# Performance work log

Measured on AMD Instinct MI355X. Metric: run time of the kernel, lower is better.

The kernel has to match this reference:

```python
import jax, jax.numpy as jnp
import numpy as np


def setup_inputs() -> dict:
    key = jax.random.key(0)
    k1, k2, k3, k4 = jax.random.split(key, 4)
    B, S, DIN, DOUT = 4, 4096, 512, 128
    x = jax.random.normal(k1, (B, S, DIN), dtype=jnp.float32)
    Wq = jax.random.normal(k2, (DIN, DOUT), dtype=jnp.float32) * 0.02
    Wk = jax.random.normal(k3, (DIN, DOUT), dtype=jnp.float32) * 0.02
    Wv = jax.random.normal(k4, (DIN, DOUT), dtype=jnp.float32) * 0.02
    return {"x": x, "Wq": Wq, "Wk": Wk, "Wv": Wv}


def reference(x, Wq, Wk, Wv):
    # x: [B, S, d_in]; projections (bias-free Linear)
    q = jnp.einsum('bsd,de->bse', x, Wq)  # [B, S, d_out]
    k = jnp.einsum('bsd,de->bse', x, Wk)
    v = jnp.einsum('bsd,de->bse', x, Wv)
    d_out = k.shape[-1]
    scores = jnp.einsum('bqe,bke->bqk', q, k) / jnp.sqrt(jnp.float32(d_out))  # [B, S, S]
    S = x.shape[1]
    causal = jnp.tril(jnp.ones((S, S), dtype=bool))  # True where attending allowed
    scores = jnp.where(causal[None], scores, jnp.float32(-jnp.inf))
    attn = jax.nn.softmax(scores, axis=-1)
    # dropout p=0.0 -> identity (eval mode)
    return jnp.einsum('bqk,bke->bqe', attn, v)  # [B, S, d_out]
```

## Files before the change

### kernel.cpp

```cpp
#include <hip/hip_runtime.h>

typedef __bf16 bf16x8 __attribute__((ext_vector_type(8)));
typedef float f32x4 __attribute__((ext_vector_type(4)));
typedef unsigned short u16;
typedef unsigned int u32;
typedef u16 u16x8 __attribute__((ext_vector_type(8)));
typedef u16 u16x4 __attribute__((ext_vector_type(4)));
typedef u32 u32x4 __attribute__((ext_vector_type(4)));

__device__ __forceinline__ u16 f2bf(float f) {
    u32 u = __builtin_bit_cast(u32, f);
    u += 0x7fffu + ((u >> 16) & 1u);
    return (u16)(u >> 16);
}
__device__ __forceinline__ float bf2f(u16 v) {
    return __builtin_bit_cast(float, (u32)v << 16);
}
__device__ __forceinline__ u32 cvtpk(float a, float b) {
    u32 d;
    asm("v_cvt_pk_bf16_f32 %0, %1, %2" : "=v"(d) : "v"(a), "v"(b));
    return d;
}
__device__ __forceinline__ f32x4 mfma16(u16x8 a, u16x8 b, f32x4 c) {
    return __builtin_amdgcn_mfma_f32_16x16x32_bf16(
        __builtin_bit_cast(bf16x8, a), __builtin_bit_cast(bf16x8, b), c, 0, 0, 0);
}

#define GLOAD16(SRC, DST)                                                     \
    __builtin_amdgcn_global_load_lds(                                         \
        (const __attribute__((address_space(1))) unsigned int*)(SRC),         \
        (__attribute__((address_space(3))) unsigned int*)(DST), 16, 0, 0)

__device__ __forceinline__ int ldsAddr(int r, int c) {
    return r * 128 + (((c >> 3) ^ (r & 7)) << 3) + (c & 7);
}

__global__ __launch_bounds__(256) void prep_all(
    const float* __restrict__ x,
    const float* __restrict__ Wq, const float* __restrict__ Wk,
    const float* __restrict__ Wv,
    u16* __restrict__ xf, u16* __restrict__ wf)
{
    __shared__ u16 T[16 * 512];
    const int t = threadIdx.x;
    if (blockIdx.x < 1024) {
        const int rb = blockIdx.x;
        const int row = t >> 4, colb = (t & 15) * 32;
        const float* src = x + (size_t)(rb * 16 + row) * 512 + colb;
        #pragma unroll
        for (int i = 0; i < 4; ++i) {
            float4 va = *(const float4*)(src + i * 8);
            float4 vb = *(const float4*)(src + i * 8 + 4);
            u16x8 v;
            v[0] = f2bf(va.x); v[1] = f2bf(va.y); v[2] = f2bf(va.z); v[3] = f2bf(va.w);
            v[4] = f2bf(vb.x); v[5] = f2bf(vb.y); v[6] = f2bf(vb.z); v[7] = f2bf(vb.w);
            int chunk = ((colb >> 3) + i) ^ (row & 7);
            *(u16x8*)&T[row * 512 + chunk * 8] = v;
        }
        __syncthreads();
        #pragma unroll
        for (int ii = 0; ii < 4; ++ii) {
            int flatF = ii * 256 + t;
            int ds = flatF >> 6, lane = flatF & 63;
            int l16 = lane & 15, g = lane >> 4;
            int chunk = (4 * ds + g) ^ (l16 & 7);
            u16x8 v = *(const u16x8*)&T[l16 * 512 + chunk * 8];
            *(u16x8*)&xf[(((size_t)rb * 16 + ds) * 64 + lane) * 8] = v;
        }
    } else {
        int flat = (blockIdx.x - 1024) * 256 + t;
        int widx = flat >> 13, rem = flat & 8191;
        int n = rem >> 10, ds = (rem >> 6) & 15, lane = rem & 63;
        int l16 = lane & 15, g = lane >> 4;
        const float* W = (widx == 0) ? Wq : (widx == 1 ? Wk : Wv);
        const float sc = (widx == 0) ? (0.08838834764831845f * 1.4426950408889634f) : 1.0f;
        u16x8 v;
        #pragma unroll
        for (int j = 0; j < 8; ++j)
            v[j] = f2bf(W[(size_t)(ds * 32 + 8 * g + j) * 128 + n * 16 + l16] * sc);
        *(u16x8*)&wf[(size_t)flat * 8] = v;
    }
}

__global__ __launch_bounds__(256, 3) void qkv2(
    const u16* __restrict__ xf, const u16* __restrict__ wf,
    u16* __restrict__ Qf, u16* __restrict__ Kf, u16* __restrict__ Vf)
{
    __shared__ u16 T4[4][16 * 128];
    const int tid = threadIdx.x, lane = tid & 63, wid = tid >> 6;
    const int g = lane >> 4, l16 = lane & 15;
    const int widx = blockIdx.y;
    const int rbg = blockIdx.x * 4 + wid;
    const u16* WfB = wf + (size_t)widx * 8192 * 8;
    u16* T = T4[wid];

    const f32x4 fz = {0.f, 0.f, 0.f, 0.f};
    f32x4 acc[8];
    #pragma unroll
    for (int n = 0; n < 8; ++n) acc[n] = fz;

    #pragma unroll 4
    for (int ds = 0; ds < 16; ++ds) {
        u16x8 a = *(const u16x8*)&xf[(((size_t)rbg * 16 + ds) * 64 + lane) * 8];
        #pragma unroll
        for (int n = 0; n < 8; ++n) {
            u16x8 b = *(const u16x8*)&WfB[((size_t)(n * 16 + ds) * 64 + lane) * 8];
            acc[n] = mfma16(a, b, acc[n]);
        }
    }

    #pragma unroll
    for (int n = 0; n < 8; ++n) {
        #pragma unroll
        for (int r = 0; r < 4; ++r)
            T[ldsAddr(4 * g + r, n * 16 + l16)] = f2bf(acc[n][r]);
    }
    if (widx < 2) {
        u16* dst = (widx == 0) ? Qf : Kf;
        #pragma unroll
        for (int ds = 0; ds < 4; ++ds) {
            int chunk = (4 * ds + g) ^ (l16 & 7);
            u16x8 v = *(const u16x8*)&T[l16 * 128 + chunk * 8];
            *(u16x8*)&dst[(((size_t)rbg * 4 + ds) * 64 + lane) * 8] = v;
        }
    } else {
        const int kb = rbg >> 2, ksel = (rbg >> 1) & 1, g0 = (rbg & 1) * 2;
        #pragma unroll
        for (int s = 0; s < 4; ++s) {
            int flat = s * 64 + lane;
            int e = flat >> 5, gg = (flat >> 4) & 1, l16p = flat & 15;
            u16x8 v;
            #pragma unroll
            for (int j = 0; j < 8; ++j)
                v[j] = T[ldsAddr(8 * gg + j, e * 16 + l16p)];
            *(u16x8*)&Vf[((((size_t)kb * 2 + ksel) * 8 + e) * 64
                          + (g0 + gg) * 16 + l16p) * 8] = v;
        }
    }
}

__global__ __launch_bounds__(256, 2) void attn6(
    const u16* __restrict__ Qf, const u16* __restrict__ Kf,
    const u16* __restrict__ Vf, float* __restrict__ out,
    u16* __restrict__ po, float* __restrict__ pml, int split)
{
    __shared__ u16 lds[2][16384];
    const int tid = threadIdx.x, lane = tid & 63, wid = tid >> 6;
    const int g = lane >> 4, l16 = lane & 15;

    int b, qb, c, u;
    if (split) {
        const int xcd = blockIdx.x & 7;
        b = xcd >> 1;
        int jb = 271 - ((xcd & 1) * 136 + (blockIdx.x >> 3));
        u = 0;
        while ((u + 1) * (u + 2) <= jb) ++u;
        int r = jb - u * (u + 1);
        int hi = (r >= u + 1) ? 1 : 0;
        qb = 2 * u + hi;
        c = r - hi * (u + 1);
    } else {
        b = blockIdx.x & 3;
        qb = blockIdx.x >> 2;
        c = 0; u = 0;
    }
    const int q0 = qb * 128 + wid * 32;
    const int k_lo = c * 256;
    const int k_hi = min(k_lo + (split ? 256 : 4096), qb * 128 + 128);
    const int nch = u + 1;
    const int wklen = q0 + 32;

    {
        const u16* src;
        if (wid < 2) src = Kf + (size_t)(b * 256 + (k_lo >> 4)) * 2048 + wid * 4096;
        else         src = Vf + (size_t)(b * 64 + (k_lo >> 6)) * 8192 + (wid - 2) * 4096;
        u16* dst = &lds[0][wid * 4096];
        #pragma unroll
        for (int j = 0; j < 8; ++j)
            GLOAD16(src + j * 512 + lane * 8, dst + j * 512);
    }
    const int rbq = b * 256 + qb * 8 + wid * 2;
    u16x8 qf0[4], qf1[4];
    #pragma unroll
    for (int ds = 0; ds < 4; ++ds) {
        qf0[ds] = *(const u16x8*)&Qf[(((size_t)rbq * 4 + ds) * 64 + lane) * 8];
        qf1[ds] = *(const u16x8*)&Qf[(((size_t)(rbq + 1) * 4 + ds) * 64 + lane) * 8];
    }

    const f32x4 fz = {0.f, 0.f, 0.f, 0.f};
    f32x4 o0[8], o1[8];
    #pragma unroll
    for (int e = 0; e < 8; ++e) { o0[e] = fz; o1[e] = fz; }
    float l0 = 0.f, l1 = 0.f;

    const int srcA = l16 + ((g & 1) << 5);
    const int srcB = srcA + 16;
    const bool hiSel = (g >= 2);

    __syncthreads();

    int bufsel = 0;
    for (int k0 = k_lo; k0 < k_hi; k0 += 64) {
        if (k0 + 64 < k_hi) {
            const u16* src;
            if (wid < 2) src = Kf + (size_t)(b * 256 + ((k0 + 64) >> 4)) * 2048 + wid * 4096;
            else         src = Vf + (size_t)(b * 64 + ((k0 + 64) >> 6)) * 8192 + (wid - 2) * 4096;
            u16* dst = &lds[bufsel ^ 1][wid * 4096];
            #pragma unroll
            for (int j = 0; j < 8; ++j)
                GLOAD16(src + j * 512 + lane * 8, dst + j * 512);
        }
        if (k0 < wklen) {
            const u16* Kl = &lds[bufsel][0];
            const u16* Vl = &lds[bufsel][8192];
            f32x4 st0[4], st1[4];
            __builtin_amdgcn_s_setprio(1);
            #pragma unroll
            for (int kt = 0; kt < 4; ++kt) {
                st0[kt] = fz; st1[kt] = fz;
                #pragma unroll
                for (int ds = 0; ds < 4; ++ds) {
                    u16x8 kf = *(const u16x8*)&Kl[(kt * 4 + ds) * 512 + lane * 8];
                    st0[kt] = mfma16(kf, qf0[ds], st0[kt]);
                    st1[kt] = mfma16(kf, qf1[ds], st1[kt]);
                }
            }
            __builtin_amdgcn_s_setprio(0);
            if (k0 + 63 > q0) {
                int qg = q0 + l16;
                #pragma unroll
                for (int kt = 0; kt < 4; ++kt)
                    #pragma unroll
                    for (int r = 0; r < 4; ++r)
                        if (k0 + kt * 16 + g * 4 + r > qg) st0[kt][r] = -1e30f;
            }
            if (k0 + 63 > q0 + 16) {
                int qg = q0 + 16 + l16;
                #pragma unroll
                for (int kt = 0; kt < 4; ++kt)
                    #pragma unroll
                    for (int r = 0; r < 4; ++r)
                        if (k0 + kt * 16 + g * 4 + r > qg) st1[kt][r] = -1e30f;
            }
            u32 pk0[4][2], pk1[4][2];
            #pragma unroll
            for (int kt = 0; kt < 4; ++kt) {
                float p0 = exp2f(st0[kt][0]), p1 = exp2f(st0[kt][1]);
                float p2 = exp2f(st0[kt][2]), p3 = exp2f(st0[kt][3]);
                l0 += (p0 + p1) + (p2 + p3);
                pk0[kt][0] = cvtpk(p0, p1);
                pk0[kt][1] = cvtpk(p2, p3);
                float q0v = exp2f(st1[kt][0]), q1v = exp2f(st1[kt][1]);
                float q2v = exp2f(st1[kt][2]), q3v = exp2f(st1[kt][3]);
                l1 += (q0v + q1v) + (q2v + q3v);
                pk1[kt][0] = cvtpk(q0v, q1v);
                pk1[kt][1] = cvtpk(q2v, q3v);
            }
            #pragma unroll
            for (int ksel = 0; ksel < 2; ++ksel) {
                u32 a0 = __shfl((int)pk0[2 * ksel][0], srcA), b0 = __shfl((int)pk0[2 * ksel + 1][0], srcA);
                u32 a1 = __shfl((int)pk0[2 * ksel][1], srcA), b1 = __shfl((int)pk0[2 * ksel + 1][1], srcA);
                u32 a2 = __shfl((int)pk0[2 * ksel][0], srcB), b2 = __shfl((int)pk0[2 * ksel + 1][0], srcB);
                u32 a3 = __shfl((int)pk0[2 * ksel][1], srcB), b3 = __shfl((int)pk0[2 * ksel + 1][1], srcB);
                u32x4 d0 = { hiSel ? b0 : a0, hiSel ? b1 : a1, hiSel ? b2 : a2, hiSel ? b3 : a3 };
                u16x8 pf0 = __builtin_bit_cast(u16x8, d0);
                u32 c0 = __shfl((int)pk1[2 * ksel][0], srcA), e0 = __shfl((int)pk1[2 * ksel + 1][0], srcA);
                u32 c1 = __shfl((int)pk1[2 * ksel][1], srcA), e1 = __shfl((int)pk1[2 * ksel + 1][1], srcA);
                u32 c2 = __shfl((int)pk1[2 * ksel][0], srcB), e2 = __shfl((int)pk1[2 * ksel + 1][0], srcB);
                u32 c3 = __shfl((int)pk1[2 * ksel][1], srcB), e3 = __shfl((int)pk1[2 * ksel + 1][1], srcB);
                u32x4 d1 = { hiSel ? e0 : c0, hiSel ? e1 : c1, hiSel ? e2 : c2, hiSel ? e3 : c3 };
                u16x8 pf1 = __builtin_bit_cast(u16x8, d1);
                __builtin_amdgcn_s_setprio(1);
                #pragma unroll
                for (int e = 0; e < 8; ++e) {
                    u16x8 vf = *(const u16x8*)&Vl[(ksel * 8 + e) * 512 + lane * 8];
                    o0[e] = mfma16(vf, pf0, o0[e]);
                    o1[e] = mfma16(vf, pf1, o1[e]);
                }
                __builtin_amdgcn_s_setprio(0);
            }
        }
        __syncthreads();
        bufsel ^= 1;
    }

    l0 += __shfl_xor(l0, 16); l0 += __shfl_xor(l0, 32);
    l1 += __shfl_xor(l1, 16); l1 += __shfl_xor(l1, 32);

    if (nch == 1) {
        float inv0 = 1.0f / l0, inv1 = 1.0f / l1;
        float* op0 = out + ((size_t)b * 4096 + q0 + l16) * 128;
        float* op1 = out + ((size_t)b * 4096 + q0 + 16 + l16) * 128;
        #pragma unroll
        for (int e = 0; e < 8; ++e) {
            f32x4 v0 = o0[e], v1 = o1[e];
            #pragma unroll
            for (int r = 0; r < 4; ++r) { v0[r] *= inv0; v1[r] *= inv1; }
            *(f32x4*)&op0[e * 16 + g * 4] = v0;
            *(f32x4*)&op1[e * 16 + g * 4] = v1;
        }
    } else {
        const int slot = b * 272 + u * (u + 1) + (qb & 1) * (u + 1) + c;
        u16* pp0 = po + ((size_t)slot * 128 + wid * 32 + l16) * 128;
        u16* pp1 = pp0 + 16 * 128;
        #pragma unroll
        for (int e = 0; e < 8; ++e) {
            u16x4 v0, v1;
            #pragma unroll
            for (int r = 0; r < 4; ++r) { v0[r] = f2bf(o0[e][r]); v1[r] = f2bf(o1[e][r]); }
            *(u16x4*)&pp0[e * 16 + g * 4] = v0;
            *(u16x4*)&pp1[e * 16 + g * 4] = v1;
        }
        if (g == 0) {
            pml[(size_t)slot * 128 + wid * 32 + l16] = l0;
            pml[(size_t)slot * 128 + wid * 32 + 16 + l16] = l1;
        }
    }
}

__global__ __launch_bounds__(256) void merge6(
    const u16* __restrict__ po, const float* __restrict__ pml,
    float* __restrict__ out)
{
    int gid = blockIdx.x * 256 + threadIdx.x;
    int colg = gid & 31;
    int rowid = gid >> 5;
    int b = rowid / 3840;
    int rr = rowid - b * 3840;
    int qb = (rr >> 7) + 2;
    int qr = rr & 127;
    int u = qb >> 1;
    int nch = u + 1;
    int slot0 = b * 272 + u * (u + 1) + (qb & 1) * (u + 1);

    float den = 0.f;
    f32x4 num = {0.f, 0.f, 0.f, 0.f};
    #pragma unroll 1
    for (int cc = 0; cc < nch; ++cc) {
        den += pml[(size_t)(slot0 + cc) * 128 + qr];
        u16x4 pv = *(const u16x4*)&po[((size_t)(slot0 + cc) * 128 + qr) * 128 + colg * 4];
        #pragma unroll
        for (int j = 0; j < 4; ++j) num[j] += bf2f(pv[j]);
    }
    float inv = 1.0f / den;
    f32x4 res = { num[0] * inv, num[1] * inv, num[2] * inv, num[3] * inv };
    *(f32x4*)&out[((size_t)b * 4096 + qb * 128 + qr) * 128 + colg * 4] = res;
}

extern "C" void kernel_launch(void* const* d_in, const int* in_sizes, int n_in,
                              void* d_out, int out_size, void* d_ws, size_t ws_size,
                              hipStream_t stream) {
    (void)in_sizes; (void)n_in; (void)out_size;
    const float* x  = (const float*)d_in[0];
    const float* Wq = (const float*)d_in[1];
    const float* Wk = (const float*)d_in[2];
    const float* Wv = (const float*)d_in[3];
    float* out = (float*)d_out;

    u16* Qf = (u16*)d_ws;
    u16* Kf = Qf + 2097152;
    u16* Vf = Kf + 2097152;
    u16* xf = Vf + 2097152;
    u16* wf = xf + 8388608;
    u16* po = xf;
    float* pml = (float*)(po + (size_t)1088 * 128 * 128);

    const size_t fixed_b = (size_t)3 * 2097152 * 2;
    const size_t part_b  = (size_t)1088 * 128 * (128 * 2 + 4);
    const int split = (ws_size >= fixed_b + part_b) ? 1 : 0;

    prep_all<<<1120, 256, 0, stream>>>(x, Wq, Wk, Wv, xf, wf);
    qkv2<<<dim3(256, 3), 256, 0, stream>>>(xf, wf, Qf, Kf, Vf);
    attn6<<<split ? 1088 : 128, 256, 0, stream>>>(Qf, Kf, Vf, out, po, pml, split);
    if (split) merge6<<<1920, 256, 0, stream>>>(po, pml, out);
}
```

Measured before the change: 84.45 us.

## Stage QKV weights in LDS and halve attention split granularity

The QKV projection kernel now double-buffers weight fragments in shared memory with async global-to-LDS loads and prefetches the next x fragment. Before, every wave read the weights straight from global memory. The split attention kernel now uses 512-key chunks instead of 256, with a new chunk schedule (qb/4+1 chunks per query block). That cuts the attention blocks from 1088 to 576 and shrinks the partial buffers and merge work. In exchange it gives fewer blocks and a longer per-block tail, and it adds a block-wide barrier to every step of the projection loop.

```diff
diff --git a/kernel.cpp b/kernel.cpp
--- a/kernel.cpp
+++ b/kernel.cpp
@@ -86,27 +86,47 @@
     const u16* __restrict__ xf, const u16* __restrict__ wf,
     u16* __restrict__ Qf, u16* __restrict__ Kf, u16* __restrict__ Vf)
 {
+    __shared__ u16 Wbuf[2][4096];
     __shared__ u16 T4[4][16 * 128];
     const int tid = threadIdx.x, lane = tid & 63, wid = tid >> 6;
     const int g = lane >> 4, l16 = lane & 15;
     const int widx = blockIdx.y;
     const int rbg = blockIdx.x * 4 + wid;
-    const u16* WfB = wf + (size_t)widx * 8192 * 8;
+    const u16* WfB = wf + (size_t)widx * 65536;
     u16* T = T4[wid];
+
+    GLOAD16(WfB + (size_t)((wid * 16 + 0) * 64 + lane) * 8,
+            Wbuf[0] + (wid * 64 + lane) * 8);
+    GLOAD16(WfB + (size_t)(((wid + 4) * 16 + 0) * 64 + lane) * 8,
+            Wbuf[0] + ((wid + 4) * 64 + lane) * 8);
 
     const f32x4 fz = {0.f, 0.f, 0.f, 0.f};
     f32x4 acc[8];
     #pragma unroll
     for (int n = 0; n < 8; ++n) acc[n] = fz;
 
-    #pragma unroll 4
+    u16x8 a_cur = *(const u16x8*)&xf[(((size_t)rbg * 16 + 0) * 64 + lane) * 8];
+    __syncthreads();
+
+    #pragma unroll 1
     for (int ds = 0; ds < 16; ++ds) {
-        u16x8 a = *(const u16x8*)&xf[(((size_t)rbg * 16 + ds) * 64 + lane) * 8];
+        u16x8 a_next;
+        if (ds + 1 < 16) {
+            const int nds = ds + 1, bb = nds & 1;
+            GLOAD16(WfB + (size_t)((wid * 16 + nds) * 64 + lane) * 8,
+                    Wbuf[bb] + (wid * 64 + lane) * 8);
+            GLOAD16(WfB + (size_t)(((wid + 4) * 16 + nds) * 64 + lane) * 8,
+                    Wbuf[bb] + ((wid + 4) * 64 + lane) * 8);
+            a_next = *(const u16x8*)&xf[(((size_t)rbg * 16 + nds) * 64 + lane) * 8];
+        }
+        const u16* Wl = Wbuf[ds & 1];
         #pragma unroll
         for (int n = 0; n < 8; ++n) {
-            u16x8 b = *(const u16x8*)&WfB[((size_t)(n * 16 + ds) * 64 + lane) * 8];
-            acc[n] = mfma16(a, b, acc[n]);
-        }
+            u16x8 b = *(const u16x8*)&Wl[(n * 64 + lane) * 8];
+            acc[n] = mfma16(a_cur, b, acc[n]);
+        }
+        __syncthreads();
+        if (ds + 1 < 16) a_cur = a_next;
     }
 
     #pragma unroll
@@ -148,26 +168,25 @@
     const int tid = threadIdx.x, lane = tid & 63, wid = tid >> 6;
     const int g = lane >> 4, l16 = lane & 15;
 
-    int b, qb, c, u;
+    int b, qb, c, nch, jb;
     if (split) {
         const int xcd = blockIdx.x & 7;
         b = xcd >> 1;
-        int jb = 271 - ((xcd & 1) * 136 + (blockIdx.x >> 3));
-        u = 0;
-        while ((u + 1) * (u + 2) <= jb) ++u;
-        int r = jb - u * (u + 1);
-        int hi = (r >= u + 1) ? 1 : 0;
-        qb = 2 * u + hi;
-        c = r - hi * (u + 1);
+        jb = 143 - ((xcd & 1) * 72 + (blockIdx.x >> 3));
+        int base = 0;
+        qb = 0;
+        #pragma unroll 1
+        while (base + ((qb + 4) >> 2) <= jb) { base += (qb + 4) >> 2; ++qb; }
+        c = jb - base;
+        nch = (qb + 4) >> 2;
     } else {
         b = blockIdx.x & 3;
         qb = blockIdx.x >> 2;
-        c = 0; u = 0;
+        c = 0; nch = 1; jb = 0;
     }
     const int q0 = qb * 128 + wid * 32;
-    const int k_lo = c * 256;
-    const int k_hi = min(k_lo + (split ? 256 : 4096), qb * 128 + 128);
-    const int nch = u + 1;
+    const int k_lo = c * 512;
+    const int k_hi = min(k_lo + (split ? 512 : 4096), qb * 128 + 128);
     const int wklen = q0 + 32;
 
     {
@@ -300,7 +319,7 @@
             *(f32x4*)&op1[e * 16 + g * 4] = v1;
         }
     } else {
-        const int slot = b * 272 + u * (u + 1) + (qb & 1) * (u + 1) + c;
+        const int slot = b * 144 + jb;
         u16* pp0 = po + ((size_t)slot * 128 + wid * 32 + l16) * 128;
         u16* pp1 = pp0 + 16 * 128;
         #pragma unroll
@@ -325,13 +344,13 @@
     int gid = blockIdx.x * 256 + threadIdx.x;
     int colg = gid & 31;
     int rowid = gid >> 5;
-    int b = rowid / 3840;
-    int rr = rowid - b * 3840;
-    int qb = (rr >> 7) + 2;
+    int b = rowid / 3584;
+    int rr = rowid - b * 3584;
+    int qb = (rr >> 7) + 4;
     int qr = rr & 127;
-    int u = qb >> 1;
-    int nch = u + 1;
-    int slot0 = b * 272 + u * (u + 1) + (qb & 1) * (u + 1);
+    int q = qb >> 2, r = qb & 3;
+    int nch = (qb + 4) >> 2;
+    int slot0 = b * 144 + 2 * q * (q + 1) + r * (q + 1);
 
     float den = 0.f;
     f32x4 num = {0.f, 0.f, 0.f, 0.f};
@@ -363,14 +382,16 @@
     u16* xf = Vf + 2097152;
     u16* wf = xf + 8388608;
     u16* po = xf;
-    float* pml = (float*)(po + (size_t)1088 * 128 * 128);
+    float* pml = (float*)(po + (size_t)576 * 128 * 128);
 
     const size_t fixed_b = (size_t)3 * 2097152 * 2;
-    const size_t part_b  = (size_t)1088 * 128 * (128 * 2 + 4);
-    const int split = (ws_size >= fixed_b + part_b) ? 1 : 0;
+    const size_t prep_b  = (size_t)(8388608 + 196608) * 2;
+    const size_t part_b  = (size_t)576 * 128 * (128 * 2 + 4);
+    const size_t scratch = part_b > prep_b ? part_b : prep_b;
+    const int split = (ws_size >= fixed_b + scratch) ? 1 : 0;
 
     prep_all<<<1120, 256, 0, stream>>>(x, Wq, Wk, Wv, xf, wf);
     qkv2<<<dim3(256, 3), 256, 0, stream>>>(xf, wf, Qf, Kf, Vf);
-    attn6<<<split ? 1088 : 128, 256, 0, stream>>>(Qf, Kf, Vf, out, po, pml, split);
-    if (split) merge6<<<1920, 256, 0, stream>>>(po, pml, out);
-}
+    attn6<<<split ? 576 : 128, 256, 0, stream>>>(Qf, Kf, Vf, out, po, pml, split);
+    if (split) merge6<<<1792, 256, 0, stream>>>(po, pml, out);
+}
```

Measured after the change: 81.14 us. 3.9% less time.

## Stage QKV weights through LDS, halve attention K tile, coalesce partial writes

Applied to the files above, without the earlier changes.

The QKV projection kernel now double-buffers the weight fragments for each K-step in shared memory using async global-to-LDS loads, and prefetches the next x fragment instead of reading weights directly from global memory. The attention kernel processes 32-key tiles instead of 64, halving its LDS footprint and raising launch bounds to 4 blocks per CU for more occupancy. Partial outputs are transposed through LDS with an XOR swizzle so they can be written with 16-byte coalesced stores. The trade-offs are more barriers per K-step and more loop iterations with less work each in the attention loop.

```diff
diff --git a/kernel.cpp b/kernel.cpp
--- a/kernel.cpp
+++ b/kernel.cpp
@@ -86,27 +86,47 @@
     const u16* __restrict__ xf, const u16* __restrict__ wf,
     u16* __restrict__ Qf, u16* __restrict__ Kf, u16* __restrict__ Vf)
 {
+    __shared__ u16 Wbuf[2][4096];
     __shared__ u16 T4[4][16 * 128];
     const int tid = threadIdx.x, lane = tid & 63, wid = tid >> 6;
     const int g = lane >> 4, l16 = lane & 15;
     const int widx = blockIdx.y;
     const int rbg = blockIdx.x * 4 + wid;
-    const u16* WfB = wf + (size_t)widx * 8192 * 8;
+    const u16* WfB = wf + (size_t)widx * 65536;
     u16* T = T4[wid];
+
+    GLOAD16(WfB + (size_t)((wid * 16 + 0) * 64 + lane) * 8,
+            Wbuf[0] + (wid * 64 + lane) * 8);
+    GLOAD16(WfB + (size_t)(((wid + 4) * 16 + 0) * 64 + lane) * 8,
+            Wbuf[0] + ((wid + 4) * 64 + lane) * 8);
 
     const f32x4 fz = {0.f, 0.f, 0.f, 0.f};
     f32x4 acc[8];
     #pragma unroll
     for (int n = 0; n < 8; ++n) acc[n] = fz;
 
-    #pragma unroll 4
+    u16x8 a_cur = *(const u16x8*)&xf[(((size_t)rbg * 16 + 0) * 64 + lane) * 8];
+    __syncthreads();
+
+    #pragma unroll 1
     for (int ds = 0; ds < 16; ++ds) {
-        u16x8 a = *(const u16x8*)&xf[(((size_t)rbg * 16 + ds) * 64 + lane) * 8];
+        u16x8 a_next;
+        if (ds + 1 < 16) {
+            const int nds = ds + 1, bb = nds & 1;
+            GLOAD16(WfB + (size_t)((wid * 16 + nds) * 64 + lane) * 8,
+                    Wbuf[bb] + (wid * 64 + lane) * 8);
+            GLOAD16(WfB + (size_t)(((wid + 4) * 16 + nds) * 64 + lane) * 8,
+                    Wbuf[bb] + ((wid + 4) * 64 + lane) * 8);
+            a_next = *(const u16x8*)&xf[(((size_t)rbg * 16 + nds) * 64 + lane) * 8];
+        }
+        const u16* Wl = Wbuf[ds & 1];
         #pragma unroll
         for (int n = 0; n < 8; ++n) {
-            u16x8 b = *(const u16x8*)&WfB[((size_t)(n * 16 + ds) * 64 + lane) * 8];
-            acc[n] = mfma16(a, b, acc[n]);
-        }
+            u16x8 b = *(const u16x8*)&Wl[(n * 64 + lane) * 8];
+            acc[n] = mfma16(a_cur, b, acc[n]);
+        }
+        __syncthreads();
+        if (ds + 1 < 16) a_cur = a_next;
     }
 
     #pragma unroll
@@ -139,12 +159,12 @@
     }
 }
 
-__global__ __launch_bounds__(256, 2) void attn6(
+__global__ __launch_bounds__(256, 4) void attn7(
     const u16* __restrict__ Qf, const u16* __restrict__ Kf,
     const u16* __restrict__ Vf, float* __restrict__ out,
     u16* __restrict__ po, float* __restrict__ pml, int split)
 {
-    __shared__ u16 lds[2][16384];
+    __shared__ u16 lds[2][8192];
     const int tid = threadIdx.x, lane = tid & 63, wid = tid >> 6;
     const int g = lane >> 4, l16 = lane & 15;
 
@@ -171,12 +191,17 @@
     const int wklen = q0 + 32;
 
     {
-        const u16* src;
-        if (wid < 2) src = Kf + (size_t)(b * 256 + (k_lo >> 4)) * 2048 + wid * 4096;
-        else         src = Vf + (size_t)(b * 64 + (k_lo >> 6)) * 8192 + (wid - 2) * 4096;
-        u16* dst = &lds[0][wid * 4096];
-        #pragma unroll
-        for (int j = 0; j < 8; ++j)
+        const u16* src; u16* dst;
+        if (wid < 2) {
+            src = Kf + (size_t)(b * 256 + (k_lo >> 4) + wid) * 2048;
+            dst = &lds[0][wid * 2048];
+        } else {
+            src = Vf + (size_t)(b * 64 + (k_lo >> 6)) * 8192
+                     + ((k_lo >> 5) & 1) * 4096 + (wid - 2) * 2048;
+            dst = &lds[0][4096 + (wid - 2) * 2048];
+        }
+        #pragma unroll
+        for (int j = 0; j < 4; ++j)
             GLOAD16(src + j * 512 + lane * 8, dst + j * 512);
     }
     const int rbq = b * 256 + qb * 8 + wid * 2;
@@ -200,23 +225,29 @@
     __syncthreads();
 
     int bufsel = 0;
-    for (int k0 = k_lo; k0 < k_hi; k0 += 64) {
-        if (k0 + 64 < k_hi) {
-            const u16* src;
-            if (wid < 2) src = Kf + (size_t)(b * 256 + ((k0 + 64) >> 4)) * 2048 + wid * 4096;
-            else         src = Vf + (size_t)(b * 64 + ((k0 + 64) >> 6)) * 8192 + (wid - 2) * 4096;
-            u16* dst = &lds[bufsel ^ 1][wid * 4096];
-            #pragma unroll
-            for (int j = 0; j < 8; ++j)
+    for (int k0 = k_lo; k0 < k_hi; k0 += 32) {
+        if (k0 + 32 < k_hi) {
+            const int kn = k0 + 32;
+            const u16* src; u16* dst;
+            if (wid < 2) {
+                src = Kf + (size_t)(b * 256 + (kn >> 4) + wid) * 2048;
+                dst = &lds[bufsel ^ 1][wid * 2048];
+            } else {
+                src = Vf + (size_t)(b * 64 + (kn >> 6)) * 8192
+                         + ((kn >> 5) & 1) * 4096 + (wid - 2) * 2048;
+                dst = &lds[bufsel ^ 1][4096 + (wid - 2) * 2048];
+            }
+            #pragma unroll
+            for (int j = 0; j < 4; ++j)
                 GLOAD16(src + j * 512 + lane * 8, dst + j * 512);
         }
         if (k0 < wklen) {
             const u16* Kl = &lds[bufsel][0];
-            const u16* Vl = &lds[bufsel][8192];
-            f32x4 st0[4], st1[4];
+            const u16* Vl = &lds[bufsel][4096];
+            f32x4 st0[2], st1[2];
             __builtin_amdgcn_s_setprio(1);
             #pragma unroll
-            for (int kt = 0; kt < 4; ++kt) {
+            for (int kt = 0; kt < 2; ++kt) {
                 st0[kt] = fz; st1[kt] = fz;
                 #pragma unroll
                 for (int ds = 0; ds < 4; ++ds) {
@@ -226,25 +257,25 @@
                 }
             }
             __builtin_amdgcn_s_setprio(0);
-            if (k0 + 63 > q0) {
+            if (k0 + 31 > q0) {
                 int qg = q0 + l16;
                 #pragma unroll
-                for (int kt = 0; kt < 4; ++kt)
+                for (int kt = 0; kt < 2; ++kt)
                     #pragma unroll
                     for (int r = 0; r < 4; ++r)
                         if (k0 + kt * 16 + g * 4 + r > qg) st0[kt][r] = -1e30f;
             }
-            if (k0 + 63 > q0 + 16) {
+            if (k0 + 31 > q0 + 16) {
                 int qg = q0 + 16 + l16;
                 #pragma unroll
-                for (int kt = 0; kt < 4; ++kt)
+                for (int kt = 0; kt < 2; ++kt)
                     #pragma unroll
                     for (int r = 0; r < 4; ++r)
                         if (k0 + kt * 16 + g * 4 + r > qg) st1[kt][r] = -1e30f;
             }
-            u32 pk0[4][2], pk1[4][2];
-            #pragma unroll
-            for (int kt = 0; kt < 4; ++kt) {
+            u32 pk0[2][2], pk1[2][2];
+            #pragma unroll
+            for (int kt = 0; kt < 2; ++kt) {
                 float p0 = exp2f(st0[kt][0]), p1 = exp2f(st0[kt][1]);
                 float p2 = exp2f(st0[kt][2]), p3 = exp2f(st0[kt][3]);
                 l0 += (p0 + p1) + (p2 + p3);
@@ -256,24 +287,24 @@
                 pk1[kt][0] = cvtpk(q0v, q1v);
                 pk1[kt][1] = cvtpk(q2v, q3v);
             }
-            #pragma unroll
-            for (int ksel = 0; ksel < 2; ++ksel) {
-                u32 a0 = __shfl((int)pk0[2 * ksel][0], srcA), b0 = __shfl((int)pk0[2 * ksel + 1][0], srcA);
-                u32 a1 = __shfl((int)pk0[2 * ksel][1], srcA), b1 = __shfl((int)pk0[2 * ksel + 1][1], srcA);
-                u32 a2 = __shfl((int)pk0[2 * ksel][0], srcB), b2 = __shfl((int)pk0[2 * ksel + 1][0], srcB);
-                u32 a3 = __shfl((int)pk0[2 * ksel][1], srcB), b3 = __shfl((int)pk0[2 * ksel + 1][1], srcB);
+            {
+                u32 a0 = __shfl((int)pk0[0][0], srcA), b0 = __shfl((int)pk0[1][0], srcA);
+                u32 a1 = __shfl((int)pk0[0][1], srcA), b1 = __shfl((int)pk0[1][1], srcA);
+                u32 a2 = __shfl((int)pk0[0][0], srcB), b2 = __shfl((int)pk0[1][0], srcB);
+                u32 a3 = __shfl((int)pk0[0][1], srcB), b3 = __shfl((int)pk0[1][1], srcB);
                 u32x4 d0 = { hiSel ? b0 : a0, hiSel ? b1 : a1, hiSel ? b2 : a2, hiSel ? b3 : a3 };
                 u16x8 pf0 = __builtin_bit_cast(u16x8, d0);
-                u32 c0 = __shfl((int)pk1[2 * ksel][0], srcA), e0 = __shfl((int)pk1[2 * ksel + 1][0], srcA);
-                u32 c1 = __shfl((int)pk1[2 * ksel][1], srcA), e1 = __shfl((int)pk1[2 * ksel + 1][1], srcA);
-                u32 c2 = __shfl((int)pk1[2 * ksel][0], srcB), e2 = __shfl((int)pk1[2 * ksel + 1][0], srcB);
-                u32 c3 = __shfl((int)pk1[2 * ksel][1], srcB), e3 = __shfl((int)pk1[2 * ksel + 1][1], srcB);
+                u32 c0 = __shfl((int)pk1[0][0], srcA), e0 = __shfl((int)pk1[1][0], srcA);
+                u32 c1 = __shfl((int)pk1[0][1], srcA), e1 = __shfl((int)pk1[1][1], srcA);
+                u32 c2 = __shfl((int)pk1[0][0], srcB), e2 = __shfl((int)pk1[1][0], srcB);
+                u32 c3 = __shfl((int)pk1[0][1], srcB), e3 = __shfl((int)pk1[1][1], srcB);
                 u32x4 d1 = { hiSel ? e0 : c0, hiSel ? e1 : c1, hiSel ? e2 : c2, hiSel ? e3 : c3 };
                 u16x8 pf1 = __builtin_bit_cast(u16x8, d1);
                 __builtin_amdgcn_s_setprio(1);
                 #pragma unroll
                 for (int e = 0; e < 8; ++e) {
-                    u16x8 vf = *(const u16x8*)&Vl[(ksel * 8 + e) * 512 + lane * 8];
+                    u16x8 vf = *(const u16x8*)&Vl[(e * 64 + lane) * 8 - e * 512 + e * 512];
+                    vf = *(const u16x8*)&Vl[e * 512 + lane * 8];
                     o0[e] = mfma16(vf, pf0, o0[e]);
                     o1[e] = mfma16(vf, pf1, o1[e]);
                 }
@@ -301,15 +332,25 @@
         }
     } else {
         const int slot = b * 272 + u * (u + 1) + (qb & 1) * (u + 1) + c;
-        u16* pp0 = po + ((size_t)slot * 128 + wid * 32 + l16) * 128;
-        u16* pp1 = pp0 + 16 * 128;
+        u16* Tw = &lds[0][0] + wid * 4096;
         #pragma unroll
         for (int e = 0; e < 8; ++e) {
             u16x4 v0, v1;
             #pragma unroll
             for (int r = 0; r < 4; ++r) { v0[r] = f2bf(o0[e][r]); v1[r] = f2bf(o1[e][r]); }
-            *(u16x4*)&pp0[e * 16 + g * 4] = v0;
-            *(u16x4*)&pp1[e * 16 + g * 4] = v1;
+            int col = e * 16 + g * 4;
+            int r0 = l16, r1 = 16 + l16;
+            *(u16x4*)&Tw[r0 * 128 + ((((col >> 3) ^ (r0 & 7)) << 3) + (col & 7))] = v0;
+            *(u16x4*)&Tw[r1 * 128 + ((((col >> 3) ^ (r1 & 7)) << 3) + (col & 7))] = v1;
+        }
+        u16* pw = po + ((size_t)slot * 128 + wid * 32) * 128;
+        #pragma unroll
+        for (int j = 0; j < 8; ++j) {
+            int idx = j * 512 + lane * 8;
+            int row = idx >> 7;
+            int chunk = (idx & 127) >> 3;
+            u16x8 v = *(const u16x8*)&Tw[(row << 7) + ((chunk ^ (row & 7)) << 3)];
+            *(u16x8*)&pw[idx] = v;
         }
         if (g == 0) {
             pml[(size_t)slot * 128 + wid * 32 + l16] = l0;
@@ -371,6 +412,6 @@
 
     prep_all<<<1120, 256, 0, stream>>>(x, Wq, Wk, Wv, xf, wf);
     qkv2<<<dim3(256, 3), 256, 0, stream>>>(xf, wf, Qf, Kf, Vf);
-    attn6<<<split ? 1088 : 128, 256, 0, stream>>>(Qf, Kf, Vf, out, po, pml, split);
+    attn7<<<split ? 1088 : 128, 256, 0, stream>>>(Qf, Kf, Vf, out, po, pml, split);
     if (split) merge6<<<1920, 256, 0, stream>>>(po, pml, out);
 }
```

New measurement: 115.8 us. 1.37x slower.
